# Performance work log

Hardware: AMD Instinct MI355X
Metric: run time of the kernel (lower is better)

The kernel has to match this reference:

```python
import jax, jax.numpy as jnp
import numpy as np

N, T, U, D, V = 8, 200, 100, 512, 500


def setup_inputs() -> dict:
    key = jax.random.key(0)
    k1, k2, k3, k4 = jax.random.split(key, 4)
    encoder_out = jax.random.normal(k1, (N, T, D), dtype=jnp.float32)
    decoder_out = jax.random.normal(k2, (N, U, D), dtype=jnp.float32)
    # nn.Linear(input_dim, output_dim): weight (V, D), bias (V,)
    bound = 1.0 / np.sqrt(D)
    W = jax.random.uniform(k3, (V, D), minval=-bound, maxval=bound, dtype=jnp.float32)
    b = jax.random.uniform(k4, (V,), minval=-bound, maxval=bound, dtype=jnp.float32)
    return {"encoder_out": encoder_out, "decoder_out": decoder_out, "W": W, "b": b}


def reference(encoder_out, decoder_out, W, b):
    # broadcast add: (N,T,1,D) + (N,1,U,D) -> (N,T,U,D)
    x = encoder_out[:, :, None, :] + decoder_out[:, None, :, :]
    activations = jnp.tanh(x)
    # linear: (N,T,U,D) @ (D,V) + b -> (N,T,U,V)
    logits = jnp.einsum("ntud,vd->ntuv", activations, W) + b
    return logits
```

## Files before the change

kernel.cpp:

```cpp
#include <hip/hip_runtime.h>
#include <hip/hip_bf16.h>


#define NB 8
#define TT 200
#define UU 100
#define DD 512
#define VV 500
#define VP 512
#define BM 64
#define BNB 256
#define BK 32
#define KSTEPS 16
#define THREADS 256
#define LDA 40
#define LCH 264
#define MROWS (NB*TT*UU)
#define MBLOCKS (MROWS/BM)

typedef __attribute__((ext_vector_type(4))) float         f32x4;
typedef __attribute__((ext_vector_type(8))) short         s16x8;
typedef __attribute__((ext_vector_type(4))) unsigned int  u32x4;

#define RAW_BAR() do { asm volatile("s_waitcnt lgkmcnt(0)" ::: "memory"); \
                       __builtin_amdgcn_s_barrier(); } while (0)

__device__ __forceinline__ unsigned short f2bf(float f) {
    unsigned int u = __builtin_bit_cast(unsigned int, f);
    u = (u + 0x7FFFu + ((u >> 16) & 1u)) >> 16;
    return (unsigned short)u;
}

__device__ __forceinline__ unsigned int cvt_pk_bf16(float a, float b) {
    unsigned int r;
    asm("v_cvt_pk_bf16_f32 %0, %1, %2" : "=v"(r) : "v"(a), "v"(b));
    return r;
}

__device__ __forceinline__ float fast_tanh(float x) {
    float e = __builtin_amdgcn_exp2f(x * 2.88539008177793f);
    return __builtin_fmaf(-2.0f, __builtin_amdgcn_rcpf(e + 1.0f), 1.0f);
}

__global__ void prep_w(const float* __restrict__ W, unsigned short* __restrict__ Wt) {
    int idx = blockIdx.x * 256 + threadIdx.x;
    int k = idx & 511;
    int v = idx >> 9;
    float val = (v < VV) ? W[v * DD + k] : 0.0f;
    Wt[(k >> 5) * (VP * BK) + v * BK + (k & 31)] = f2bf(val);
}

#define KBODY(kc, CUR, NXT, BC, BNX)                                          \
  {                                                                           \
       \
    if ((kc) < KSTEPS - 1) {                                                  \
      _Pragma("unroll")                                                       \
      for (int f = 0; f < 4; ++f)                                             \
        BNX[f] = *(const s16x8*)(wptr + ((kc)+1) * (VP * BK) + f * (16*BK));  \
    }                                                                         \
                                               \
    s16x8 aF[4];                                                              \
    _Pragma("unroll")                                                         \
    for (int m = 0; m < 4; ++m)                                               \
      aF[m] = *(const s16x8*)(&CUR[(m * 16 + lr) * LDA + lk * 8]);            \
                     \
    if ((kc) < KSTEPS - 1) {                                                  \
      u32x4 wds;                                                              \
      wds[0] = cvt_pk_bf16(fast_tanh(e0[0]+d0[0]), fast_tanh(e0[1]+d0[1]));   \
      wds[1] = cvt_pk_bf16(fast_tanh(e0[2]+d0[2]), fast_tanh(e0[3]+d0[3]));   \
      wds[2] = cvt_pk_bf16(fast_tanh(e1[0]+d1[0]), fast_tanh(e1[1]+d1[1]));   \
      wds[3] = cvt_pk_bf16(fast_tanh(e1[2]+d1[2]), fast_tanh(e1[3]+d1[3]));   \
      *(u32x4*)(&NXT[srow * LDA + sk]) = wds;                                 \
      if ((kc) < KSTEPS - 2) {                                                \
        const float* e2 = ep + ((kc)+2) * BK;                                 \
        const float* d2 = dp + ((kc)+2) * BK;                                 \
        e0 = *(const f32x4*)(e2);  e1 = *(const f32x4*)(e2 + 4);              \
        d0 = *(const f32x4*)(d2);  d1 = *(const f32x4*)(d2 + 4);              \
      }                                                                       \
    }                                                                         \
                        \
    __builtin_amdgcn_s_setprio(1);                                            \
    _Pragma("unroll")                                                         \
    for (int m = 0; m < 4; ++m)                                               \
      _Pragma("unroll")                                                       \
      for (int f = 0; f < 4; ++f)                                             \
        acc[m][f] = __builtin_amdgcn_mfma_f32_16x16x32_bf16(aF[m], BC[f],     \
                                                            acc[m][f],0,0,0); \
    __builtin_amdgcn_s_setprio(0);                                            \
                \
    if ((kc) < KSTEPS - 1) RAW_BAR();                                         \
  }

__global__ __launch_bounds__(THREADS, 3) void joiner_kernel(
    const float* __restrict__ enc, const float* __restrict__ dec,
    const unsigned short* __restrict__ Wt, const float* __restrict__ bias,
    float* __restrict__ out)
{
    __shared__ __align__(16) char smem[16 * LCH * 4];
    unsigned short* lA0 = (unsigned short*)smem;
    unsigned short* lA1 = (unsigned short*)(smem + BM * LDA * 2);

    const int tid  = threadIdx.x;
    const int mb   = blockIdx.x;
    const int vb   = blockIdx.y;
    const int lane = tid & 63;
    const int wn   = tid >> 6;
    const int lr   = lane & 15;
    const int lk   = lane >> 4;

    const int srow = tid >> 2;
    const int sk   = (tid & 3) << 3;

    int r   = mb * BM + srow;
    int n   = r / (TT * UU);
    int rem = r - n * (TT * UU);
    int t   = rem / UU;
    int u   = rem - t * UU;
    const float* ep = enc + (n * TT + t) * DD + sk;
    const float* dp = dec + (n * UU + u) * DD + sk;

    const unsigned short* wptr = Wt + (vb * BNB + wn * 64 + lr) * BK + lk * 8;

    f32x4 e0, e1, d0, d1;
    s16x8 b0[4], b1[4];

    e0 = *(const f32x4*)(ep);     e1 = *(const f32x4*)(ep + 4);
    d0 = *(const f32x4*)(dp);     d1 = *(const f32x4*)(dp + 4);
    #pragma unroll
    for (int f = 0; f < 4; ++f)
        b0[f] = *(const s16x8*)(wptr + f * (16 * BK));
    {
        u32x4 wds;
        wds[0] = cvt_pk_bf16(fast_tanh(e0[0]+d0[0]), fast_tanh(e0[1]+d0[1]));
        wds[1] = cvt_pk_bf16(fast_tanh(e0[2]+d0[2]), fast_tanh(e0[3]+d0[3]));
        wds[2] = cvt_pk_bf16(fast_tanh(e1[0]+d1[0]), fast_tanh(e1[1]+d1[1]));
        wds[3] = cvt_pk_bf16(fast_tanh(e1[2]+d1[2]), fast_tanh(e1[3]+d1[3]));
        *(u32x4*)(&lA0[srow * LDA + sk]) = wds;
    }
    e0 = *(const f32x4*)(ep + BK);     e1 = *(const f32x4*)(ep + BK + 4);
    d0 = *(const f32x4*)(dp + BK);     d1 = *(const f32x4*)(dp + BK + 4);
    RAW_BAR();

    f32x4 acc[4][4];
    #pragma unroll
    for (int m = 0; m < 4; ++m)
        #pragma unroll
        for (int f = 0; f < 4; ++f)
            acc[m][f] = (f32x4){0.f, 0.f, 0.f, 0.f};

    #pragma unroll
    for (int kk = 0; kk < KSTEPS; kk += 2) {
        KBODY(kk,     lA0, lA1, b0, b1)
        KBODY(kk + 1, lA1, lA0, b1, b0)
    }

    float bv[4];
    #pragma unroll
    for (int f = 0; f < 4; ++f) {
        int v = vb * BNB + wn * 64 + f * 16 + lr;
        bv[f] = (v < VV) ? bias[v] : 0.0f;
    }

    float* lchunk = (float*)smem;
    const int slabcols = (vb == 0) ? BNB : (VV - BNB);
    const int segmax   = slabcols >> 2;
    float* outbase = out + (long)mb * BM * VV + vb * BNB;

    for (int c = 0; c < 4; ++c) {
        RAW_BAR();
        #pragma unroll
        for (int f = 0; f < 4; ++f) {
            int vloc = wn * 64 + f * 16 + lr;
            #pragma unroll
            for (int q = 0; q < 4; ++q)
                lchunk[(lk * 4 + q) * LCH + vloc] = acc[c][f][q] + bv[f];
        }
        RAW_BAR();
        float* dst = outbase + c * 16 * VV;
        #pragma unroll
        for (int i = 0; i < 4; ++i) {
            int idx = i * THREADS + tid;
            int row = idx >> 6;
            int seg = idx & 63;
            if (seg < segmax)
                *(f32x4*)(dst + row * VV + seg * 4) =
                    *(const f32x4*)(lchunk + row * LCH + seg * 4);
        }
    }
}

extern "C" void kernel_launch(void* const* d_in, const int* in_sizes, int n_in,
                              void* d_out, int out_size, void* d_ws, size_t ws_size,
                              hipStream_t stream) {
    const float* enc = (const float*)d_in[0];
    const float* dec = (const float*)d_in[1];
    const float* W   = (const float*)d_in[2];
    const float* b   = (const float*)d_in[3];
    float* out = (float*)d_out;
    unsigned short* Wt = (unsigned short*)d_ws;

    prep_w<<<dim3((VP * DD) / 256), dim3(256), 0, stream>>>(W, Wt);
    joiner_kernel<<<dim3(MBLOCKS, 2), dim3(THREADS), 0, stream>>>(enc, dec, Wt, b, out);
}
```

Measured before the change: 151.1 us.

## Stage full-K activation tile in LDS once and sweep both vocab halves

The block tile shrinks to 32 rows and the whole 32x512 tanh activation tile is computed once into swizzled LDS. Both 256-column vocab halves are then swept within the same block, so the activation is not recomputed by two blocks as before. The per-k-step barrier is removed, W fragments are triple-buffered from global memory, and the launch bound rises to 4 waves per SIMD. In exchange each block uses more LDS (40 KB) and has a smaller M tile, so every W fragment is reused across fewer rows.

```diff
diff --git a/kernel.cpp b/kernel.cpp
--- a/kernel.cpp
+++ b/kernel.cpp
@@ -8,13 +8,9 @@
 #define DD 512
 #define VV 500
 #define VP 512
-#define BM 64
-#define BNB 256
+#define BM 32
 #define BK 32
-#define KSTEPS 16
 #define THREADS 256
-#define LDA 40
-#define LCH 264
 #define MROWS (NB*TT*UU)
 #define MBLOCKS (MROWS/BM)
 
@@ -50,141 +46,148 @@
     Wt[(k >> 5) * (VP * BK) + v * BK + (k & 31)] = f2bf(val);
 }
 
-#define KBODY(kc, CUR, NXT, BC, BNX)                                          \
+#define KSTEP(kc, BC_, AFC_, AFN_)                                            \
   {                                                                           \
-       \
-    if ((kc) < KSTEPS - 1) {                                                  \
+    if ((kc) < 15) {                                                          \
       _Pragma("unroll")                                                       \
-      for (int f = 0; f < 4; ++f)                                             \
-        BNX[f] = *(const s16x8*)(wptr + ((kc)+1) * (VP * BK) + f * (16*BK));  \
-    }                                                                         \
-                                               \
-    s16x8 aF[4];                                                              \
-    _Pragma("unroll")                                                         \
-    for (int m = 0; m < 4; ++m)                                               \
-      aF[m] = *(const s16x8*)(&CUR[(m * 16 + lr) * LDA + lk * 8]);            \
-                     \
-    if ((kc) < KSTEPS - 1) {                                                  \
-      u32x4 wds;                                                              \
-      wds[0] = cvt_pk_bf16(fast_tanh(e0[0]+d0[0]), fast_tanh(e0[1]+d0[1]));   \
-      wds[1] = cvt_pk_bf16(fast_tanh(e0[2]+d0[2]), fast_tanh(e0[3]+d0[3]));   \
-      wds[2] = cvt_pk_bf16(fast_tanh(e1[0]+d1[0]), fast_tanh(e1[1]+d1[1]));   \
-      wds[3] = cvt_pk_bf16(fast_tanh(e1[2]+d1[2]), fast_tanh(e1[3]+d1[3]));   \
-      *(u32x4*)(&NXT[srow * LDA + sk]) = wds;                                 \
-      if ((kc) < KSTEPS - 2) {                                                \
-        const float* e2 = ep + ((kc)+2) * BK;                                 \
-        const float* d2 = dp + ((kc)+2) * BK;                                 \
-        e0 = *(const f32x4*)(e2);  e1 = *(const f32x4*)(e2 + 4);              \
-        d0 = *(const f32x4*)(d2);  d1 = *(const f32x4*)(d2 + 4);              \
+      for (int m = 0; m < 2; ++m) {                                           \
+        int row = m * 16 + lr;                                                \
+        int swz = ((((kc)+1) * 4 + lk) ^ (lr & 7));                           \
+        AFN_[m] = *(const s16x8*)(&lA[row * 512 + swz * 8]);                  \
       }                                                                       \
     }                                                                         \
-                        \
-    __builtin_amdgcn_s_setprio(1);                                            \
     _Pragma("unroll")                                                         \
-    for (int m = 0; m < 4; ++m)                                               \
-      _Pragma("unroll")                                                       \
-      for (int f = 0; f < 4; ++f)                                             \
-        acc[m][f] = __builtin_amdgcn_mfma_f32_16x16x32_bf16(aF[m], BC[f],     \
-                                                            acc[m][f],0,0,0); \
-    __builtin_amdgcn_s_setprio(0);                                            \
-                \
-    if ((kc) < KSTEPS - 1) RAW_BAR();                                         \
+    for (int f = 0; f < 4; ++f) {                                             \
+      acc[0][f] = __builtin_amdgcn_mfma_f32_16x16x32_bf16(AFC_[0], BC_[f],    \
+                                                          acc[0][f], 0,0,0);  \
+      acc[1][f] = __builtin_amdgcn_mfma_f32_16x16x32_bf16(AFC_[1], BC_[f],    \
+                                                          acc[1][f], 0,0,0);  \
+      if ((kc) <= 12)                                                         \
+        BC_[f] = *(const s16x8*)(wptrP + ((kc)+3) * (VP * BK) + f * (16*BK)); \
+    }                                                                         \
   }
 
-__global__ __launch_bounds__(THREADS, 3) void joiner_kernel(
+__global__ __launch_bounds__(THREADS, 4) void joiner_kernel(
     const float* __restrict__ enc, const float* __restrict__ dec,
     const unsigned short* __restrict__ Wt, const float* __restrict__ bias,
     float* __restrict__ out)
 {
-    __shared__ __align__(16) char smem[16 * LCH * 4];
-    unsigned short* lA0 = (unsigned short*)smem;
-    unsigned short* lA1 = (unsigned short*)(smem + BM * LDA * 2);
+    __shared__ __align__(16) char smem[40960];
+    unsigned short* lA = (unsigned short*)smem;
+    float* lchunk = (float*)(smem + 32768);
 
     const int tid  = threadIdx.x;
     const int mb   = blockIdx.x;
-    const int vb   = blockIdx.y;
     const int lane = tid & 63;
     const int wn   = tid >> 6;
     const int lr   = lane & 15;
     const int lk   = lane >> 4;
 
-    const int srow = tid >> 2;
-    const int sk   = (tid & 3) << 3;
-
-    int r   = mb * BM + srow;
-    int n   = r / (TT * UU);
-    int rem = r - n * (TT * UU);
-    int t   = rem / UU;
-    int u   = rem - t * UU;
-    const float* ep = enc + (n * TT + t) * DD + sk;
-    const float* dp = dec + (n * UU + u) * DD + sk;
-
-    const unsigned short* wptr = Wt + (vb * BNB + wn * 64 + lr) * BK + lk * 8;
-
-    f32x4 e0, e1, d0, d1;
-    s16x8 b0[4], b1[4];
-
-    e0 = *(const f32x4*)(ep);     e1 = *(const f32x4*)(ep + 4);
-    d0 = *(const f32x4*)(dp);     d1 = *(const f32x4*)(dp + 4);
+    const int srow  = tid >> 3;
+    const int scol0 = (tid & 7) << 6;
+
+    {
+        int r   = mb * BM + srow;
+        int n   = r / (TT * UU);
+        int rem = r - n * (TT * UU);
+        int t   = rem / UU;
+        int u   = rem - t * UU;
+        const float* ep = enc + (n * TT + t) * DD + scol0;
+        const float* dp = dec + (n * UU + u) * DD + scol0;
+        #pragma unroll
+        for (int c8 = 0; c8 < 8; ++c8) {
+            f32x4 e0 = *(const f32x4*)(ep + c8 * 8);
+            f32x4 e1 = *(const f32x4*)(ep + c8 * 8 + 4);
+            f32x4 d0 = *(const f32x4*)(dp + c8 * 8);
+            f32x4 d1 = *(const f32x4*)(dp + c8 * 8 + 4);
+            u32x4 wds;
+            wds[0] = cvt_pk_bf16(fast_tanh(e0[0]+d0[0]), fast_tanh(e0[1]+d0[1]));
+            wds[1] = cvt_pk_bf16(fast_tanh(e0[2]+d0[2]), fast_tanh(e0[3]+d0[3]));
+            wds[2] = cvt_pk_bf16(fast_tanh(e1[0]+d1[0]), fast_tanh(e1[1]+d1[1]));
+            wds[3] = cvt_pk_bf16(fast_tanh(e1[2]+d1[2]), fast_tanh(e1[3]+d1[3]));
+            int slot = (scol0 >> 3) + c8;
+            int swz  = slot ^ (srow & 7);
+            *(u32x4*)(&lA[srow * 512 + swz * 8]) = wds;
+        }
+    }
+    RAW_BAR();
+
+    float* outrow = out + (long)mb * BM * VV;
+
     #pragma unroll
-    for (int f = 0; f < 4; ++f)
-        b0[f] = *(const s16x8*)(wptr + f * (16 * BK));
-    {
-        u32x4 wds;
-        wds[0] = cvt_pk_bf16(fast_tanh(e0[0]+d0[0]), fast_tanh(e0[1]+d0[1]));
-        wds[1] = cvt_pk_bf16(fast_tanh(e0[2]+d0[2]), fast_tanh(e0[3]+d0[3]));
-        wds[2] = cvt_pk_bf16(fast_tanh(e1[0]+d1[0]), fast_tanh(e1[1]+d1[1]));
-        wds[3] = cvt_pk_bf16(fast_tanh(e1[2]+d1[2]), fast_tanh(e1[3]+d1[3]));
-        *(u32x4*)(&lA0[srow * LDA + sk]) = wds;
-    }
-    e0 = *(const f32x4*)(ep + BK);     e1 = *(const f32x4*)(ep + BK + 4);
-    d0 = *(const f32x4*)(dp + BK);     d1 = *(const f32x4*)(dp + BK + 4);
-    RAW_BAR();
-
-    f32x4 acc[4][4];
-    #pragma unroll
-    for (int m = 0; m < 4; ++m)
-        #pragma unroll
-        for (int f = 0; f < 4; ++f)
-            acc[m][f] = (f32x4){0.f, 0.f, 0.f, 0.f};
-
-    #pragma unroll
-    for (int kk = 0; kk < KSTEPS; kk += 2) {
-        KBODY(kk,     lA0, lA1, b0, b1)
-        KBODY(kk + 1, lA1, lA0, b1, b0)
-    }
-
-    float bv[4];
-    #pragma unroll
-    for (int f = 0; f < 4; ++f) {
-        int v = vb * BNB + wn * 64 + f * 16 + lr;
-        bv[f] = (v < VV) ? bias[v] : 0.0f;
-    }
-
-    float* lchunk = (float*)smem;
-    const int slabcols = (vb == 0) ? BNB : (VV - BNB);
-    const int segmax   = slabcols >> 2;
-    float* outbase = out + (long)mb * BM * VV + vb * BNB;
-
-    for (int c = 0; c < 4; ++c) {
-        RAW_BAR();
+    for (int p = 0; p < 2; ++p) {
+        const unsigned short* wptrP = Wt + (p * 256 + wn * 64 + lr) * BK + lk * 8;
+
+        f32x4 acc[2][4];
+        #pragma unroll
+        for (int m = 0; m < 2; ++m)
+            #pragma unroll
+            for (int f = 0; f < 4; ++f)
+                acc[m][f] = (f32x4){0.f, 0.f, 0.f, 0.f};
+
+        s16x8 b0[4], b1[4], b2[4];
         #pragma unroll
         for (int f = 0; f < 4; ++f) {
-            int vloc = wn * 64 + f * 16 + lr;
+            b0[f] = *(const s16x8*)(wptrP + 0 * (VP * BK) + f * (16 * BK));
+            b1[f] = *(const s16x8*)(wptrP + 1 * (VP * BK) + f * (16 * BK));
+            b2[f] = *(const s16x8*)(wptrP + 2 * (VP * BK) + f * (16 * BK));
+        }
+        s16x8 af0[2], af1[2];
+        #pragma unroll
+        for (int m = 0; m < 2; ++m) {
+            int row = m * 16 + lr;
+            int swz = (lk ^ (lr & 7));
+            af0[m] = *(const s16x8*)(&lA[row * 512 + swz * 8]);
+        }
+
+        KSTEP(0,  b0, af0, af1)
+        KSTEP(1,  b1, af1, af0)
+        KSTEP(2,  b2, af0, af1)
+        KSTEP(3,  b0, af1, af0)
+        KSTEP(4,  b1, af0, af1)
+        KSTEP(5,  b2, af1, af0)
+        KSTEP(6,  b0, af0, af1)
+        KSTEP(7,  b1, af1, af0)
+        KSTEP(8,  b2, af0, af1)
+        KSTEP(9,  b0, af1, af0)
+        KSTEP(10, b1, af0, af1)
+        KSTEP(11, b2, af1, af0)
+        KSTEP(12, b0, af0, af1)
+        KSTEP(13, b1, af1, af0)
+        KSTEP(14, b2, af0, af1)
+        KSTEP(15, b0, af1, af0)
+
+        float bv[4];
+        #pragma unroll
+        for (int f = 0; f < 4; ++f) {
+            int v = p * 256 + wn * 64 + f * 16 + lr;
+            bv[f] = (v < VV) ? bias[v] : 0.0f;
+        }
+        const int segmax = (p == 0) ? 64 : 61;
+        float* outcol = outrow + p * 256;
+
+        for (int ch = 0; ch < 4; ++ch) {
+            RAW_BAR();
+            if ((lk >> 1) == (ch & 1)) {
+                int m = ch >> 1;
+                #pragma unroll
+                for (int f = 0; f < 4; ++f) {
+                    int vloc = wn * 64 + f * 16 + lr;
+                    #pragma unroll
+                    for (int q = 0; q < 4; ++q)
+                        lchunk[((lk & 1) * 4 + q) * 256 + vloc] = acc[m][f][q] + bv[f];
+                }
+            }
+            RAW_BAR();
             #pragma unroll
-            for (int q = 0; q < 4; ++q)
-                lchunk[(lk * 4 + q) * LCH + vloc] = acc[c][f][q] + bv[f];
-        }
-        RAW_BAR();
-        float* dst = outbase + c * 16 * VV;
-        #pragma unroll
-        for (int i = 0; i < 4; ++i) {
-            int idx = i * THREADS + tid;
-            int row = idx >> 6;
-            int seg = idx & 63;
-            if (seg < segmax)
-                *(f32x4*)(dst + row * VV + seg * 4) =
-                    *(const f32x4*)(lchunk + row * LCH + seg * 4);
+            for (int i = 0; i < 2; ++i) {
+                int idx = i * THREADS + tid;
+                int row = idx >> 6;
+                int seg = idx & 63;
+                if (seg < segmax)
+                    *(f32x4*)(outcol + (long)(ch * 8 + row) * VV + seg * 4) =
+                        *(const f32x4*)(lchunk + row * 256 + seg * 4);
+            }
         }
     }
 }
@@ -200,5 +203,5 @@
     unsigned short* Wt = (unsigned short*)d_ws;
 
     prep_w<<<dim3((VP * DD) / 256), dim3(256), 0, stream>>>(W, Wt);
-    joiner_kernel<<<dim3(MBLOCKS, 2), dim3(THREADS), 0, stream>>>(enc, dec, Wt, b, out);
-}
+    joiner_kernel<<<dim3(MBLOCKS), dim3(THREADS), 0, stream>>>(enc, dec, Wt, b, out);
+}
```

After: 235.3 us. 55.8% more time.
